# Kernel tuning notes

Measured on AMD Instinct MI355X. Metric: run time of the kernel, lower is better.

The kernel has to match this reference:

```python
import jax, jax.numpy as jnp
import numpy as np

B, S, IN, H = 32, 512, 512, 1024


def setup_inputs() -> dict:
    key = jax.random.key(0)
    k1, k2, k3 = jax.random.split(key, 3)
    x = jax.random.normal(k1, (B, S, IN), dtype=jnp.float32)
    # Linear weights: [4H, fan_in], init scaled like nn.Linear (~1/sqrt(fan_in))
    W0 = jax.random.normal(k2, (4 * H, IN + H), dtype=jnp.float32) * (1.0 / np.sqrt(IN + H))
    W1 = jax.random.normal(k3, (4 * H, H + H), dtype=jnp.float32) * (1.0 / np.sqrt(H + H))
    b0 = jnp.zeros((4 * H,), dtype=jnp.float32)
    b1 = jnp.zeros((4 * H,), dtype=jnp.float32)
    return {"x": x, "W0": W0, "b0": b0, "W1": W1, "b1": b1}


def _run_layer(inp, W, b):
    """Run one unidirectional LSTM layer over time with lax.scan.

    inp: [B, S, D_in]; W: [4H, D_in+H]; b: [4H].
    Returns (outputs [B, S, H], h_n [B, H], c_n [B, H]).
    """
    h_size = W.shape[0] // 4
    bsz = inp.shape[0]

    def step(carry, x_t):
        h, c = carry
        combined = jnp.concatenate([x_t, h], axis=1)          # [B, D_in+H]
        gates = combined @ W.T + b                            # [B, 4H]
        i, f, g, o = jnp.split(gates, 4, axis=1)
        i = jax.nn.sigmoid(i)
        f = jax.nn.sigmoid(f)
        g = jnp.tanh(g)
        o = jax.nn.sigmoid(o)
        c_next = f * c + i * g
        h_next = o * jnp.tanh(c_next)
        return (h_next, c_next), h_next

    h0 = jnp.zeros((bsz, h_size), dtype=inp.dtype)
    c0 = jnp.zeros((bsz, h_size), dtype=inp.dtype)
    (h_n, c_n), ys = jax.lax.scan(step, (h0, c0), jnp.swapaxes(inp, 0, 1))
    return jnp.swapaxes(ys, 0, 1), h_n, c_n


def reference(x, W0, b0, W1, b1):
    out0, h0n, c0n = _run_layer(x, W0, b0)
    out1, h1n, c1n = _run_layer(out0, W1, b1)
    h_n = jnp.stack([h0n, h1n], axis=0)   # [num_layers, B, H]
    c_n = jnp.stack([c0n, c1n], axis=0)
    return out1[:, -1, :], h_n, c_n
```

## Files before the change

kernel.cpp:

```cpp
#include <hip/hip_runtime.h>


typedef unsigned short ushort_t;
typedef unsigned long long u64_t;
typedef __attribute__((ext_vector_type(8))) short short8;
typedef __attribute__((ext_vector_type(4))) float f32x4;
typedef __attribute__((ext_vector_type(4))) unsigned uint4v;

#define NWG       256
#define NTHREADS  512
#define SEQ       512
#define HSLOT     32768
#define FULLSLOTS 513
#define ABORT_U32 8128
#define CNT_BYTES 32768
#define POLL_MAX  6000

__device__ __forceinline__ ushort_t f2bf(float f) {
  unsigned u = __builtin_bit_cast(unsigned, f);
  u += 0x7FFFu + ((u >> 16) & 1u);
  return (ushort_t)(u >> 16);
}

__device__ __forceinline__ short8 pack_bf8(f32x4 a, f32x4 b) {
  short8 r;
  r[0] = (short)f2bf(a[0]); r[1] = (short)f2bf(a[1]);
  r[2] = (short)f2bf(a[2]); r[3] = (short)f2bf(a[3]);
  r[4] = (short)f2bf(b[0]); r[5] = (short)f2bf(b[1]);
  r[6] = (short)f2bf(b[2]); r[7] = (short)f2bf(b[3]);
  return r;
}

__device__ __forceinline__ float sigm(float x) { return 1.0f / (1.0f + __expf(-x)); }
__device__ __forceinline__ float fast_tanh(float x) {
  x = fminf(fmaxf(x, -15.f), 15.f);
  float e = __expf(-2.0f * x);
  return (1.0f - e) / (1.0f + e);
}

__device__ __forceinline__ unsigned aload(const unsigned* p) {
  return __hip_atomic_load(p, __ATOMIC_RELAXED, __HIP_MEMORY_SCOPE_AGENT);
}

__device__ __forceinline__ void wg_barrier() {
  asm volatile("s_waitcnt lgkmcnt(0)" ::: "memory");
  __builtin_amdgcn_s_barrier();
  __builtin_amdgcn_sched_barrier(0);
}

template<bool COH>
__device__ __forceinline__ void load16g(f32x4* hv, const char* base) {
#pragma unroll
  for (int ch = 0; ch < 16; ++ch) {
    const char* a = base + (long)ch * 2048;
    if constexpr (COH)
      asm volatile("global_load_dwordx4 %0, %1, off sc0 sc1"
                   : "=v"(hv[ch]) : "v"(a));
    else
      asm volatile("global_load_dwordx4 %0, %1, off"
                   : "=v"(hv[ch]) : "v"(a));
  }
  asm volatile("s_waitcnt vmcnt(0)" ::: "memory");
  __builtin_amdgcn_sched_barrier(0);
}

__device__ __forceinline__ int bad16(const f32x4* hv) {
  int bad = 0;
#pragma unroll
  for (int ch = 0; ch < 16; ++ch) {
    uint4v d = __builtin_bit_cast(uint4v, hv[ch]);
    unsigned m0 = d[0] > d[1] ? d[0] : d[1];
    unsigned m1 = d[2] > d[3] ? d[2] : d[3];
    unsigned m  = m0 > m1 ? m0 : m1;
    bad |= (int)(m == 0xFFFFFFFFu);
  }
  return bad;
}

template<bool FIRSTCOH>
__device__ __forceinline__ void poll16(f32x4* hv, const char* base,
                                       unsigned* abortp) {
  load16g<FIRSTCOH>(hv, base);
  if (!__any(bad16(hv))) return;
  for (int it = 0;; ++it) {
    load16g<true>(hv, base);
    if (!__any(bad16(hv))) return;
    if ((it & 63) == 63 && aload(abortp) != 0) return;
    if (it >= POLL_MAX) {
      __hip_atomic_store(abortp, 1u, __ATOMIC_RELAXED, __HIP_MEMORY_SCOPE_AGENT);
      return;
    }
    if (it > 8) __builtin_amdgcn_s_sleep(2);
  }
}

template<int KX, bool XFP32, bool ISL1>
__device__ __forceinline__ void run_layer(
    const void* xsrc, long x_step, long x_bstride,
    const ushort_t* __restrict__ hbuf, ushort_t* __restrict__ hbuf_w,
    const float* __restrict__ W, int ldw,
    const float* __restrict__ bias,
    float* __restrict__ out, int out_h_off, int out_c_off, int write_last,
    float* xbuf, float* red, unsigned* abortp, int ub)
{
  constexpr int XCH = (KX / 2) / 32;
  const int lane  = threadIdx.x & 63;
  const int wave  = threadIdx.x >> 6;
  const int ntile = wave >> 2;
  const int r     = wave & 3;
  const bool isH  = r < 2;
  const int sub   = r & 1;
  const int wrow  = lane & 15;
  const int kg    = lane >> 4;
  const int koff  = kg * 8;
  const int bb    = ntile * 16 + (lane & 15);

  const int kbase = isH ? (KX + sub * 512) : ((r - 2) * (KX / 2));
  const int mych  = isH ? 16 : XCH;
  short8 wreg[2][16];
  #pragma unroll
  for (int mt = 0; mt < 2; ++mt) {
    const int grow = (wrow & 3) * 1024 + ub + mt * 4 + (wrow >> 2);
    const float* ws = W + (long)grow * ldw + kbase + koff;
    #pragma unroll
    for (int ch = 0; ch < 16; ++ch) {
      if (ch < mych) {
        f32x4 v0 = *(const f32x4*)(ws + ch * 32);
        f32x4 v1 = *(const f32x4*)(ws + ch * 32 + 4);
        wreg[mt][ch] = pack_bf8(v0, v1);
      }
    }
  }

  const int u0 = ub + kg;
  float bI[2], bF[2], bG[2], bO[2], c[2] = {0.f, 0.f};
  #pragma unroll
  for (int mt = 0; mt < 2; ++mt) {
    const int u = u0 + mt * 4;
    bI[mt] = bias[u];        bF[mt] = bias[1024 + u];
    bG[mt] = bias[2048 + u]; bO[mt] = bias[3072 + u];
  }

  for (int w = 0; w <= SEQ; ++w) {
    const int t = w - 1;
    f32x4 acc[2] = {{0.f,0.f,0.f,0.f},{0.f,0.f,0.f,0.f}};

    if (isH && w >= 1) {
      const char* gb = (const char*)hbuf + (long)t * (HSLOT * 2)
                     + (long)(((sub * 64 + kg) * 32 + bb) * 16);
      f32x4 hv[16];
      poll16<true>(hv, gb, abortp);
      f32x4 accB[2] = {{0.f,0.f,0.f,0.f},{0.f,0.f,0.f,0.f}};
      #pragma unroll
      for (int ch = 0; ch < 16; ch += 2) {
        short8 b0 = __builtin_bit_cast(short8, hv[ch]);
        short8 b1 = __builtin_bit_cast(short8, hv[ch + 1]);
        acc[0]  = __builtin_amdgcn_mfma_f32_16x16x32_bf16(wreg[0][ch],   b0, acc[0], 0, 0, 0);
        acc[1]  = __builtin_amdgcn_mfma_f32_16x16x32_bf16(wreg[1][ch],   b0, acc[1], 0, 0, 0);
        accB[0] = __builtin_amdgcn_mfma_f32_16x16x32_bf16(wreg[0][ch+1], b1, accB[0], 0, 0, 0);
        accB[1] = __builtin_amdgcn_mfma_f32_16x16x32_bf16(wreg[1][ch+1], b1, accB[1], 0, 0, 0);
      }
      acc[0] += accB[0];
      acc[1] += accB[1];
      if (sub == 0) {
        #pragma unroll
        for (int mt = 0; mt < 2; ++mt)
          *(f32x4*)&red[((ntile * 2 + mt) * 64 + lane) * 4] = acc[mt];
      }
    }

    wg_barrier();

    if (isH && sub == 1 && w >= 1) {
      u64_t pk[2]; float hh[2];
      #pragma unroll
      for (int mt = 0; mt < 2; ++mt) {
        f32x4 a = acc[mt];
        a += *(const f32x4*)&red[((ntile * 2 + mt) * 64 + lane) * 4];
        a += *(const f32x4*)&xbuf[(((((t & 1) * 2 + ntile) * 2 + 0) * 2 + mt) * 64 + lane) * 4];
        a += *(const f32x4*)&xbuf[(((((t & 1) * 2 + ntile) * 2 + 1) * 2 + mt) * 64 + lane) * 4];
        float pi = a[0] + bI[mt], pf = a[1] + bF[mt];
        float pg = a[2] + bG[mt], po = a[3] + bO[mt];
        float ig = sigm(pi), fg = sigm(pf), gg = fast_tanh(pg), og = sigm(po);
        c[mt] = fg * c[mt] + ig * gg;
        float h = og * fast_tanh(c[mt]);
        hh[mt] = h;
        unsigned v  = f2bf(h);
        unsigned v1 = __shfl((int)v, (lane & 15) + 16);
        unsigned v2 = __shfl((int)v, (lane & 15) + 32);
        unsigned v3 = __shfl((int)v, (lane & 15) + 48);
        pk[mt] = (u64_t)(v & 0xFFFFu) | ((u64_t)(v1 & 0xFFFFu) << 16)
               | ((u64_t)(v2 & 0xFFFFu) << 32) | ((u64_t)(v3 & 0xFFFFu) << 48);
      }
      if (t == SEQ - 1) {
        #pragma unroll
        for (int mt = 0; mt < 2; ++mt) {
          const int u = u0 + mt * 4;
          out[out_h_off + bb * 1024 + u] = hh[mt];
          out[out_c_off + bb * 1024 + u] = c[mt];
          if (write_last) out[bb * 1024 + u] = hh[mt];
        }
      }
      if (lane < 16) {
        u64_t* dst = (u64_t*)((char*)hbuf_w + (long)(t + 1) * (HSLOT * 2)
                              + (long)((((ub >> 3) * 32 + bb)) * 16));
        __hip_atomic_store(dst,     pk[0], __ATOMIC_RELAXED, __HIP_MEMORY_SCOPE_AGENT);
        __hip_atomic_store(dst + 1, pk[1], __ATOMIC_RELAXED, __HIP_MEMORY_SCOPE_AGENT);
      }
    }

    if (!isH && w < SEQ) {
      const int s = w;
      f32x4 xa[2]  = {{0.f,0.f,0.f,0.f},{0.f,0.f,0.f,0.f}};
      f32x4 xaB[2] = {{0.f,0.f,0.f,0.f},{0.f,0.f,0.f,0.f}};
      if constexpr (XFP32) {
        const float* bp = (const float*)xsrc + (long)s * x_step
                          + (long)bb * x_bstride + kbase + koff;
        f32x4 xv[2 * XCH];
        #pragma unroll
        for (int ch = 0; ch < XCH; ++ch) {
          xv[2*ch]   = *(const f32x4*)(bp + ch * 32);
          xv[2*ch+1] = *(const f32x4*)(bp + ch * 32 + 4);
        }
        #pragma unroll
        for (int ch = 0; ch < XCH; ch += 2) {
          short8 bf0 = pack_bf8(xv[2*ch],   xv[2*ch+1]);
          short8 bf1 = pack_bf8(xv[2*ch+2], xv[2*ch+3]);
          xa[0]  = __builtin_amdgcn_mfma_f32_16x16x32_bf16(wreg[0][ch],   bf0, xa[0], 0, 0, 0);
          xa[1]  = __builtin_amdgcn_mfma_f32_16x16x32_bf16(wreg[1][ch],   bf0, xa[1], 0, 0, 0);
          xaB[0] = __builtin_amdgcn_mfma_f32_16x16x32_bf16(wreg[0][ch+1], bf1, xaB[0], 0, 0, 0);
          xaB[1] = __builtin_amdgcn_mfma_f32_16x16x32_bf16(wreg[1][ch+1], bf1, xaB[1], 0, 0, 0);
        }
      } else {
        const char* gb = (const char*)xsrc + (long)s * (HSLOT * 2)
                       + (long)((((r - 2) * 64 + kg) * 32 + bb) * 16);
        f32x4 xv[16];
        poll16<false>(xv, gb, abortp);
        #pragma unroll
        for (int ch = 0; ch < 16; ch += 2) {
          short8 b0 = __builtin_bit_cast(short8, xv[ch]);
          short8 b1 = __builtin_bit_cast(short8, xv[ch + 1]);
          xa[0]  = __builtin_amdgcn_mfma_f32_16x16x32_bf16(wreg[0][ch],   b0, xa[0], 0, 0, 0);
          xa[1]  = __builtin_amdgcn_mfma_f32_16x16x32_bf16(wreg[1][ch],   b0, xa[1], 0, 0, 0);
          xaB[0] = __builtin_amdgcn_mfma_f32_16x16x32_bf16(wreg[0][ch+1], b1, xaB[0], 0, 0, 0);
          xaB[1] = __builtin_amdgcn_mfma_f32_16x16x32_bf16(wreg[1][ch+1], b1, xaB[1], 0, 0, 0);
        }
      }
      xa[0] += xaB[0];
      xa[1] += xaB[1];
      #pragma unroll
      for (int mt = 0; mt < 2; ++mt)
        *(f32x4*)&xbuf[(((((s & 1) * 2 + ntile) * 2 + (r - 2)) * 2 + mt) * 64 + lane) * 4] = xa[mt];
    }

    wg_barrier();
  }
}

__global__ __launch_bounds__(NTHREADS, 2)
void lstm_persistent(const float* __restrict__ x,  const float* __restrict__ W0,
                     const float* __restrict__ b0, const float* __restrict__ W1,
                     const float* __restrict__ b1, float* __restrict__ out,
                     unsigned* cnt, ushort_t* O0, ushort_t* H1)
{
  __shared__ float xbuf[4096];
  __shared__ float red[1024];
  const int role = (int)(blockIdx.x >> 7);
  const int ub   = (int)(blockIdx.x & 127) * 8;
  unsigned* abortp = cnt + ABORT_U32;

  if (role == 0) {
    run_layer<512, true, false>(x, 512, 262144,
                                O0, O0, W0, 1536, b0,
                                out, 32768, 98304, 0,
                                xbuf, red, abortp, ub);
  } else {
    run_layer<1024, false, true>((const void*)(O0 + HSLOT), HSLOT, 1024,
                                 H1, H1, W1, 2048, b1,
                                 out, 65536, 131072, 1,
                                 xbuf, red, abortp, ub);
  }
}

extern "C" void kernel_launch(void* const* d_in, const int* in_sizes, int n_in,
                              void* d_out, int out_size, void* d_ws, size_t ws_size,
                              hipStream_t stream) {
  (void)in_sizes; (void)n_in; (void)out_size;

  const float* x  = (const float*)d_in[0];
  const float* W0 = (const float*)d_in[1];
  const float* b0 = (const float*)d_in[2];
  const float* W1 = (const float*)d_in[3];
  const float* b1 = (const float*)d_in[4];
  float* out = (float*)d_out;

  const size_t hb_bytes = (size_t)FULLSLOTS * HSLOT * sizeof(ushort_t);
  const size_t need     = CNT_BYTES + 2 * hb_bytes;
  if (ws_size < need) return;

  unsigned* cnt = (unsigned*)d_ws;
  ushort_t* O0  = (ushort_t*)((char*)d_ws + CNT_BYTES);
  ushort_t* H1  = O0 + (size_t)FULLSLOTS * HSLOT;

  hipMemsetAsync(cnt, 0, CNT_BYTES, stream);
  hipMemsetAsync(O0, 0x00, (size_t)HSLOT * 2, stream);
  hipMemsetAsync(O0 + HSLOT, 0xFF, (size_t)(FULLSLOTS - 1) * HSLOT * 2, stream);
  hipMemsetAsync(H1, 0x00, (size_t)HSLOT * 2, stream);
  hipMemsetAsync(H1 + HSLOT, 0xFF, (size_t)(FULLSLOTS - 1) * HSLOT * 2, stream);

  lstm_persistent<<<dim3(NWG), dim3(NTHREADS), 0, stream>>>(
      x, W0, b0, W1, b1, out, cnt, O0, H1);
}
```

Baseline: 2.058 ms.

## Gate hidden-state reads on striped arrival counters instead of sentinel polling

Adds per-layer striped atomic counters that each workgroup bumps after publishing its hidden-state slice. Readers spin on these 16 counter stripes before issuing plain (non-coherent) loads of the h buffer, instead of repeatedly reloading the whole 16-chunk slot with coherent loads and checking for sentinel values. The aim is to cut polling traffic on the big buffer, at the cost of an extra vmcnt drain, an LDS atomic and a global atomic per step on the critical recurrence path. The poll timeout is also raised.

```diff
diff --git a/kernel.cpp b/kernel.cpp
--- a/kernel.cpp
+++ b/kernel.cpp
@@ -12,9 +12,10 @@
 #define SEQ       512
 #define HSLOT     32768
 #define FULLSLOTS 513
+#define LBASE     4096
 #define ABORT_U32 8128
 #define CNT_BYTES 32768
-#define POLL_MAX  6000
+#define POLL_MAX  20000
 
 __device__ __forceinline__ ushort_t f2bf(float f) {
   unsigned u = __builtin_bit_cast(unsigned, f);
@@ -46,6 +47,23 @@
   asm volatile("s_waitcnt lgkmcnt(0)" ::: "memory");
   __builtin_amdgcn_s_barrier();
   __builtin_amdgcn_sched_barrier(0);
+}
+
+__device__ __forceinline__ void gate_stripes(const unsigned* stripes,
+                                             unsigned target,
+                                             unsigned* abortp) {
+  if (target == 0u) return;
+  const int lane = threadIdx.x & 63;
+  const unsigned* addr = stripes + (lane & 15) * 16;
+  for (int it = 0;; ++it) {
+    unsigned v = aload(addr);
+    if (__all((int)(v >= target))) return;
+    if ((it & 63) == 63 && aload(abortp) != 0) return;
+    if (it >= POLL_MAX) {
+      __hip_atomic_store(abortp, 1u, __ATOMIC_RELAXED, __HIP_MEMORY_SCOPE_AGENT);
+      return;
+    }
+  }
 }
 
 template<bool COH>
@@ -77,10 +95,9 @@
   return bad;
 }
 
-template<bool FIRSTCOH>
-__device__ __forceinline__ void poll16(f32x4* hv, const char* base,
+__device__ __forceinline__ void read16(f32x4* hv, const char* base,
                                        unsigned* abortp) {
-  load16g<FIRSTCOH>(hv, base);
+  load16g<false>(hv, base);
   if (!__any(bad16(hv))) return;
   for (int it = 0;; ++it) {
     load16g<true>(hv, base);
@@ -101,7 +118,9 @@
     const float* __restrict__ W, int ldw,
     const float* __restrict__ bias,
     float* __restrict__ out, int out_h_off, int out_c_off, int write_last,
-    float* xbuf, float* red, unsigned* abortp, int ub)
+    float* xbuf, float* red, unsigned* hcount,
+    unsigned* cntOwn, unsigned* cntOther, unsigned* abortp,
+    int lidx, int ub)
 {
   constexpr int XCH = (KX / 2) / 32;
   const int lane  = threadIdx.x & 63;
@@ -146,10 +165,11 @@
     f32x4 acc[2] = {{0.f,0.f,0.f,0.f},{0.f,0.f,0.f,0.f}};
 
     if (isH && w >= 1) {
+      gate_stripes(cntOwn, 8u * (unsigned)t, abortp);
       const char* gb = (const char*)hbuf + (long)t * (HSLOT * 2)
                      + (long)(((sub * 64 + kg) * 32 + bb) * 16);
       f32x4 hv[16];
-      poll16<true>(hv, gb, abortp);
+      read16(hv, gb, abortp);
       f32x4 accB[2] = {{0.f,0.f,0.f,0.f},{0.f,0.f,0.f,0.f}};
       #pragma unroll
       for (int ch = 0; ch < 16; ch += 2) {
@@ -207,6 +227,13 @@
         __hip_atomic_store(dst,     pk[0], __ATOMIC_RELAXED, __HIP_MEMORY_SCOPE_AGENT);
         __hip_atomic_store(dst + 1, pk[1], __ATOMIC_RELAXED, __HIP_MEMORY_SCOPE_AGENT);
       }
+      asm volatile("s_waitcnt vmcnt(0)" ::: "memory");
+      int dr = 0;
+      if (lane == 0) dr = (int)(atomicAdd(hcount, 1u) & 1u);
+      dr = __shfl(dr, 0);
+      if (dr && lane == 0)
+        __hip_atomic_fetch_add(cntOwn + (lidx & 15) * 16, 1u,
+                               __ATOMIC_RELAXED, __HIP_MEMORY_SCOPE_AGENT);
     }
 
     if (!isH && w < SEQ) {
@@ -232,10 +259,11 @@
           xaB[1] = __builtin_amdgcn_mfma_f32_16x16x32_bf16(wreg[1][ch+1], bf1, xaB[1], 0, 0, 0);
         }
       } else {
+        gate_stripes(cntOther, 8u * (unsigned)(s + 1), abortp);
         const char* gb = (const char*)xsrc + (long)s * (HSLOT * 2)
                        + (long)((((r - 2) * 64 + kg) * 32 + bb) * 16);
         f32x4 xv[16];
-        poll16<false>(xv, gb, abortp);
+        read16(xv, gb, abortp);
         #pragma unroll
         for (int ch = 0; ch < 16; ch += 2) {
           short8 b0 = __builtin_bit_cast(short8, xv[ch]);
@@ -265,20 +293,29 @@
 {
   __shared__ float xbuf[4096];
   __shared__ float red[1024];
+  __shared__ unsigned hcount;
   const int role = (int)(blockIdx.x >> 7);
-  const int ub   = (int)(blockIdx.x & 127) * 8;
-  unsigned* abortp = cnt + ABORT_U32;
+  const int lidx = (int)(blockIdx.x & 127);
+  const int ub   = lidx * 8;
+  unsigned* cntOwn   = cnt + role * LBASE;
+  unsigned* cntOther = cnt + (1 - role) * LBASE;
+  unsigned* abortp   = cnt + ABORT_U32;
+
+  if (threadIdx.x == 0) hcount = 0;
+  __syncthreads();
 
   if (role == 0) {
     run_layer<512, true, false>(x, 512, 262144,
                                 O0, O0, W0, 1536, b0,
                                 out, 32768, 98304, 0,
-                                xbuf, red, abortp, ub);
+                                xbuf, red, &hcount, cntOwn, cntOther, abortp,
+                                lidx, ub);
   } else {
     run_layer<1024, false, true>((const void*)(O0 + HSLOT), HSLOT, 1024,
                                  H1, H1, W1, 2048, b1,
                                  out, 65536, 131072, 1,
-                                 xbuf, red, abortp, ub);
+                                 xbuf, red, &hcount, cntOwn, cntOther, abortp,
+                                 lidx, ub);
   }
 }
 
```

Measured after the change: 3.718 ms. 80.6% more time.

## Split gate epilogue across both h-waves and re-poll only stale chunks

Applied to the files above, without the earlier changes.

The LSTM cell epilogue, previously done by one sub-wave for both m-tiles, is now split so each of the two h-waves finishes one m-tile. Each wave exchanges its partial accumulator through shared memory. This halves the serial transcendental and shuffle work on the per-step critical path. The polling loop now reloads only the chunks still marked as not-ready instead of all 16, which cuts redundant coherent loads while spinning. Both waves now write to shared memory before the barrier, adding some LDS traffic.

```diff
diff --git a/kernel.cpp b/kernel.cpp
--- a/kernel.cpp
+++ b/kernel.cpp
@@ -64,27 +64,38 @@
   __builtin_amdgcn_sched_barrier(0);
 }
 
-__device__ __forceinline__ int bad16(const f32x4* hv) {
-  int bad = 0;
+__device__ __forceinline__ unsigned badmask16(const f32x4* hv) {
+  unsigned m = 0;
 #pragma unroll
   for (int ch = 0; ch < 16; ++ch) {
     uint4v d = __builtin_bit_cast(uint4v, hv[ch]);
     unsigned m0 = d[0] > d[1] ? d[0] : d[1];
     unsigned m1 = d[2] > d[3] ? d[2] : d[3];
-    unsigned m  = m0 > m1 ? m0 : m1;
-    bad |= (int)(m == 0xFFFFFFFFu);
-  }
-  return bad;
+    unsigned mx = m0 > m1 ? m0 : m1;
+    m |= (mx == 0xFFFFFFFFu) ? (1u << ch) : 0u;
+  }
+  return m;
 }
 
 template<bool FIRSTCOH>
 __device__ __forceinline__ void poll16(f32x4* hv, const char* base,
                                        unsigned* abortp) {
   load16g<FIRSTCOH>(hv, base);
-  if (!__any(bad16(hv))) return;
+  unsigned bm = badmask16(hv);
+  if (!__any((int)(bm != 0u))) return;
   for (int it = 0;; ++it) {
-    load16g<true>(hv, base);
-    if (!__any(bad16(hv))) return;
+#pragma unroll
+    for (int ch = 0; ch < 16; ++ch) {
+      if (bm & (1u << ch)) {
+        const char* a = base + (long)ch * 2048;
+        asm volatile("global_load_dwordx4 %0, %1, off sc0 sc1"
+                     : "=v"(hv[ch]) : "v"(a));
+      }
+    }
+    asm volatile("s_waitcnt vmcnt(0)" ::: "memory");
+    __builtin_amdgcn_sched_barrier(0);
+    bm = badmask16(hv);
+    if (!__any((int)(bm != 0u))) return;
     if ((it & 63) == 63 && aload(abortp) != 0) return;
     if (it >= POLL_MAX) {
       __hip_atomic_store(abortp, 1u, __ATOMIC_RELAXED, __HIP_MEMORY_SCOPE_AGENT);
@@ -132,14 +143,10 @@
     }
   }
 
-  const int u0 = ub + kg;
-  float bI[2], bF[2], bG[2], bO[2], c[2] = {0.f, 0.f};
-  #pragma unroll
-  for (int mt = 0; mt < 2; ++mt) {
-    const int u = u0 + mt * 4;
-    bI[mt] = bias[u];        bF[mt] = bias[1024 + u];
-    bG[mt] = bias[2048 + u]; bO[mt] = bias[3072 + u];
-  }
+  const int uo = ub + kg + sub * 4;
+  const float bI = bias[uo],        bF = bias[1024 + uo];
+  const float bG = bias[2048 + uo], bO = bias[3072 + uo];
+  float cs = 0.f;
 
   for (int w = 0; w <= SEQ; ++w) {
     const int t = w - 1;
@@ -162,50 +169,37 @@
       }
       acc[0] += accB[0];
       acc[1] += accB[1];
-      if (sub == 0) {
-        #pragma unroll
-        for (int mt = 0; mt < 2; ++mt)
-          *(f32x4*)&red[((ntile * 2 + mt) * 64 + lane) * 4] = acc[mt];
-      }
+      *(f32x4*)&red[((sub * 2 + ntile) * 64 + lane) * 4] = acc[1 - sub];
     }
 
     wg_barrier();
 
-    if (isH && sub == 1 && w >= 1) {
-      u64_t pk[2]; float hh[2];
-      #pragma unroll
-      for (int mt = 0; mt < 2; ++mt) {
-        f32x4 a = acc[mt];
-        a += *(const f32x4*)&red[((ntile * 2 + mt) * 64 + lane) * 4];
-        a += *(const f32x4*)&xbuf[(((((t & 1) * 2 + ntile) * 2 + 0) * 2 + mt) * 64 + lane) * 4];
-        a += *(const f32x4*)&xbuf[(((((t & 1) * 2 + ntile) * 2 + 1) * 2 + mt) * 64 + lane) * 4];
-        float pi = a[0] + bI[mt], pf = a[1] + bF[mt];
-        float pg = a[2] + bG[mt], po = a[3] + bO[mt];
-        float ig = sigm(pi), fg = sigm(pf), gg = fast_tanh(pg), og = sigm(po);
-        c[mt] = fg * c[mt] + ig * gg;
-        float h = og * fast_tanh(c[mt]);
-        hh[mt] = h;
-        unsigned v  = f2bf(h);
-        unsigned v1 = __shfl((int)v, (lane & 15) + 16);
-        unsigned v2 = __shfl((int)v, (lane & 15) + 32);
-        unsigned v3 = __shfl((int)v, (lane & 15) + 48);
-        pk[mt] = (u64_t)(v & 0xFFFFu) | ((u64_t)(v1 & 0xFFFFu) << 16)
+    if (isH && w >= 1) {
+      const int mt = sub;
+      f32x4 a = acc[mt];
+      a += *(const f32x4*)&red[(((1 - sub) * 2 + ntile) * 64 + lane) * 4];
+      a += *(const f32x4*)&xbuf[(((((t & 1) * 2 + ntile) * 2 + 0) * 2 + mt) * 64 + lane) * 4];
+      a += *(const f32x4*)&xbuf[(((((t & 1) * 2 + ntile) * 2 + 1) * 2 + mt) * 64 + lane) * 4];
+      float pi = a[0] + bI, pf = a[1] + bF;
+      float pg = a[2] + bG, po = a[3] + bO;
+      float ig = sigm(pi), fg = sigm(pf), gg = fast_tanh(pg), og = sigm(po);
+      cs = fg * cs + ig * gg;
+      float h = og * fast_tanh(cs);
+      unsigned v  = f2bf(h);
+      unsigned v1 = __shfl((int)v, (lane & 15) + 16);
+      unsigned v2 = __shfl((int)v, (lane & 15) + 32);
+      unsigned v3 = __shfl((int)v, (lane & 15) + 48);
+      u64_t pk = (u64_t)(v & 0xFFFFu) | ((u64_t)(v1 & 0xFFFFu) << 16)
                | ((u64_t)(v2 & 0xFFFFu) << 32) | ((u64_t)(v3 & 0xFFFFu) << 48);
-      }
       if (t == SEQ - 1) {
-        #pragma unroll
-        for (int mt = 0; mt < 2; ++mt) {
-          const int u = u0 + mt * 4;
-          out[out_h_off + bb * 1024 + u] = hh[mt];
-          out[out_c_off + bb * 1024 + u] = c[mt];
-          if (write_last) out[bb * 1024 + u] = hh[mt];
-        }
+        out[out_h_off + bb * 1024 + uo] = h;
+        out[out_c_off + bb * 1024 + uo] = cs;
+        if (write_last) out[bb * 1024 + uo] = h;
       }
       if (lane < 16) {
         u64_t* dst = (u64_t*)((char*)hbuf_w + (long)(t + 1) * (HSLOT * 2)
                               + (long)((((ub >> 3) * 32 + bb)) * 16));
-        __hip_atomic_store(dst,     pk[0], __ATOMIC_RELAXED, __HIP_MEMORY_SCOPE_AGENT);
-        __hip_atomic_store(dst + 1, pk[1], __ATOMIC_RELAXED, __HIP_MEMORY_SCOPE_AGENT);
+        __hip_atomic_store(dst + sub, pk, __ATOMIC_RELAXED, __HIP_MEMORY_SCOPE_AGENT);
       }
     }
 
```

Measured after the change: 2.727 ms. 32.5% more time.
